# Optimization experiments

Measured on AMD Instinct MI355X. Metric: run time of the kernel, lower is better.

Reference implementation:

```python
import jax, jax.numpy as jnp
import numpy as np

N = 10000
E = 80000
NUM_TYPES = 1000
IN_CH = 64
EMB = 128
IN_GNN = EMB + IN_CH - 1  # 191
NUM_GRAPHS = 16
NUM_CLASSES = 2


def _glorot(key, shape):
    fan_in, fan_out = shape[0], shape[1]
    lim = jnp.sqrt(6.0 / (fan_in + fan_out))
    return jax.random.uniform(key, shape, jnp.float32, -lim, lim)


def setup_inputs() -> dict:
    key = jax.random.key(0)
    ks = jax.random.split(key, 20)
    node_type_ids = jax.random.randint(ks[0], (N,), 0, NUM_TYPES)
    other_feats = jax.random.normal(ks[1], (N, IN_CH - 1), jnp.float32)
    edge_index = jax.random.randint(ks[2], (2, E), 0, N)
    batch = jnp.sort(jax.random.randint(ks[3], (N,), 0, NUM_GRAPHS))
    params = dict(
        emb=jax.random.normal(ks[4], (NUM_TYPES, EMB), jnp.float32),
        W1=_glorot(ks[5], (IN_GNN, 2048)), b1=jnp.zeros((2048,), jnp.float32),
        W2=_glorot(ks[6], (2048, 1024)), b2=jnp.zeros((1024,), jnp.float32),
        W3=_glorot(ks[7], (1024, 1024)), b3=jnp.zeros((1024,), jnp.float32),
        h1w=_glorot(ks[8], (1024, 1024)), h1b=jnp.zeros((1024,), jnp.float32),
        h2w=_glorot(ks[9], (1024, 1024)), h2b=jnp.zeros((1024,), jnp.float32),
        h3w=_glorot(ks[10], (1024, 512)), h3b=jnp.zeros((512,), jnp.float32),
        ow=_glorot(ks[11], (512, NUM_CLASSES)), ob=jnp.zeros((NUM_CLASSES,), jnp.float32),
    )
    return dict(node_type_ids=node_type_ids, other_feats=other_feats,
                edge_index=edge_index, batch=batch, **params)


def _gcn_norm(edge_index, num_nodes):
    # add self loops + symmetric normalization D^-1/2 (A+I) D^-1/2 (PyG GCNConv defaults)
    loop = jnp.arange(num_nodes, dtype=edge_index.dtype)
    src = jnp.concatenate([edge_index[0], loop])
    dst = jnp.concatenate([edge_index[1], loop])
    deg = jax.ops.segment_sum(jnp.ones_like(src, jnp.float32), dst, num_segments=num_nodes)
    dinv = jnp.where(deg > 0, jax.lax.rsqrt(jnp.maximum(deg, 1.0)), 0.0)
    norm = dinv[src] * dinv[dst]
    return src, dst, norm


def _gcn_conv(x, src, dst, norm, W, b):
    h = x @ W                                    # [N, out] dense GEMM first (PyG order)
    msg = h[src] * norm[:, None]                 # gather + scale over edges
    agg = jax.ops.segment_sum(msg, dst, num_segments=x.shape[0])  # scatter-add
    return agg + b


def reference(node_type_ids, other_feats, edge_index, batch,
              emb, W1, b1, W2, b2, W3, b3,
              h1w, h1b, h2w, h2b, h3w, h3b, ow, ob):
    # eval mode: dropout is identity
    x = jnp.concatenate([emb[node_type_ids], other_feats], axis=-1)  # [N, 191]
    src, dst, norm = _gcn_norm(edge_index, x.shape[0])
    x = jax.nn.relu(_gcn_conv(x, src, dst, norm, W1, b1))
    x = jax.nn.relu(_gcn_conv(x, src, dst, norm, W2, b2))
    x = jax.nn.relu(_gcn_conv(x, src, dst, norm, W3, b3))
    # global mean pool over graphs
    sums = jax.ops.segment_sum(x, batch, num_segments=NUM_GRAPHS)
    cnts = jax.ops.segment_sum(jnp.ones((x.shape[0],), jnp.float32), batch, num_segments=NUM_GRAPHS)
    g = sums / jnp.maximum(cnts, 1.0)[:, None]   # [G, 1024]
    g = jax.nn.relu(g @ h1w + h1b)
    g = jax.nn.relu(g @ h2w + h2b)
    g = jax.nn.relu(g @ h3w + h3b)
    return g @ ow + ob                           # [G, num_classes]
```

## Files before the change

kernel.cpp:

```cpp
#include <hip/hip_runtime.h>


#define N_NODES 10000
#define N_EDGES 80000
#define EMB_DIM 128
#define FEAT_DIM 63
#define IN_GNN 191
#define IN_STRIDE 192
#define H1 2048
#define H2 1024
#define NGRAPH 16
#define NCLS 2
#define PCHUNK 8

using ushort = unsigned short;
typedef __attribute__((ext_vector_type(8))) short s8b;
typedef __attribute__((ext_vector_type(4))) float f4v;

__device__ __forceinline__ float us2f(ushort u) {
    union { unsigned int i; float f; } v; v.i = ((unsigned int)u) << 16; return v.f;
}
__device__ __forceinline__ ushort f2us(float f) {
    union { unsigned int i; float f; } v; v.f = f;
    unsigned int r = v.i + 0x7FFFu + ((v.i >> 16) & 1u);
    return (ushort)(r >> 16);
}
__device__ __forceinline__ float ldm(const void* p, long i, int md) {
    return (md == 1) ? us2f(((const ushort*)p)[i]) : ((const float*)p)[i];
}

__global__ void GraphV1EmbLarge_73864847556672_kernel() {}

__global__ void k_prep0(int* __restrict__ a, int na, float* __restrict__ b, int nb,
                        const ushort* __restrict__ feats, int* __restrict__ mode) {
    int i = blockIdx.x * 256 + threadIdx.x;
    if (i < na) a[i] = 0;
    if (i < nb) b[i] = 0.f;
    if (blockIdx.x == 0 && threadIdx.x == 0) {
        int sane = 0;
        for (int j = 0; j < 256; j++) {
            ushort u = feats[j];
            int e = (u >> 7) & 0xFF;
            if (u == 0 || (e >= 97 && e <= 157)) sane++;
        }
        *mode = (sane >= 220) ? 1 : 2;
    }
}

__global__ void k_deg_i(const int* __restrict__ dst, int* __restrict__ cnt) {
    int e = blockIdx.x * blockDim.x + threadIdx.x;
    if (e < N_EDGES) atomicAdd(&cnt[dst[e]], 1);
}
__global__ void k_scan(const int* __restrict__ cnt, int* __restrict__ indptr,
                       float* __restrict__ dinv) {
    __shared__ int part[256];
    int t = threadIdx.x;
    int base = t * 40;
    int s = 0;
    for (int i = 0; i < 40; i++) { int idx = base + i; if (idx < N_NODES) s += cnt[idx]; }
    part[t] = s;
    __syncthreads();
    if (t == 0) {
        int run = 0;
        for (int i = 0; i < 256; i++) { int tmp = part[i]; part[i] = run; run += tmp; }
        indptr[N_NODES] = run;
    }
    __syncthreads();
    int run = part[t];
    for (int i = 0; i < 40; i++) {
        int idx = base + i;
        if (idx < N_NODES) {
            indptr[idx] = run; run += cnt[idx];
            dinv[idx] = rsqrtf((float)cnt[idx] + 1.0f);
        }
    }
}
__global__ void k_fill(const int* __restrict__ src, const int* __restrict__ dst,
                       const int* __restrict__ indptr, int* __restrict__ cursor,
                       const float* __restrict__ dinv, int* __restrict__ ecol,
                       float* __restrict__ ewgt, const int* __restrict__ batch,
                       int* __restrict__ starts) {
    int b = blockIdx.x;
    if (b < 313) {
        int e = b * 256 + threadIdx.x;
        if (e >= N_EDGES) return;
        int d = dst[e], s = src[e];
        int slot = indptr[d] + atomicAdd(&cursor[d], 1);
        ecol[slot] = s;
        ewgt[slot] = dinv[s] * dinv[d];
    } else {
        int i = (b - 313) * 256 + threadIdx.x;
        if (i > N_NODES) return;
        int bc = (i < N_NODES) ? batch[i] : NGRAPH;
        int bp = (i == 0) ? -1 : batch[i - 1];
        for (int g = bp + 1; g <= bc; g++) starts[g] = i;
    }
}

__device__ __forceinline__ void cvt_tile(const void* W, int K, int N, int Kp,
                                         ushort* Wt, int n0, int k0, int md) {
    __shared__ float tile[32][33];
    int tx = threadIdx.x, ty = threadIdx.y;
    for (int r = ty; r < 32; r += 8) {
        int k = k0 + r;
        tile[r][tx] = (k < K) ? ldm(W, (long)k * N + n0 + tx, md) : 0.f;
    }
    __syncthreads();
    for (int r = ty; r < 32; r += 8) {
        int nn = n0 + r, kk = k0 + tx;
        if (kk < Kp) Wt[(long)nn * Kp + kk] = f2us(tile[tx][r]);
    }
}

__global__ void k_cvt_all(const void* W1, const void* W2, const void* W3,
                          const void* h1, const void* h2, const void* h3,
                          ushort* W1t, ushort* W2t, ushort* W3t,
                          ushort* h1t, ushort* h2t, ushort* h3t,
                          const int* __restrict__ types, const void* emb,
                          const void* feats, ushort* __restrict__ x0,
                          const void* b1, const void* b2, const void* b3,
                          float* __restrict__ b1f, float* __restrict__ b2f,
                          float* __restrict__ b3f, const int* __restrict__ mode) {
    int md = *mode;
    int b = blockIdx.x;
    if (b < 384) {
        int t = b;        cvt_tile(W1, IN_GNN, H1, IN_STRIDE, W1t, (t % 64) * 32, (t / 64) * 32, md);
    } else if (b < 2432) {
        int t = b - 384;  cvt_tile(W2, H1, H2, H1, W2t, (t % 32) * 32, (t / 32) * 32, md);
    } else if (b < 3456) {
        int t = b - 2432; cvt_tile(W3, H2, H2, H2, W3t, (t % 32) * 32, (t / 32) * 32, md);
    } else if (b < 4480) {
        int t = b - 3456; cvt_tile(h1, H2, H2, H2, h1t, (t % 32) * 32, (t / 32) * 32, md);
    } else if (b < 5504) {
        int t = b - 4480; cvt_tile(h2, H2, H2, H2, h2t, (t % 32) * 32, (t / 32) * 32, md);
    } else if (b < 6016) {
        int t = b - 5504; cvt_tile(h3, H2, 512, H2, h3t, (t % 16) * 32, (t / 16) * 32, md);
    } else if (b < 16016) {
        int i = b - 6016;
        int c = threadIdx.y * 32 + threadIdx.x;
        if (c >= IN_STRIDE) return;
        float v = 0.f;
        if (c < EMB_DIM) v = ldm(emb, (long)types[i] * EMB_DIM + c, md);
        else if (c < IN_GNN) v = ldm(feats, (long)i * FEAT_DIM + (c - EMB_DIM), md);
        x0[(long)i * IN_STRIDE + c] = f2us(v);
    } else {
        int i = (b - 16016) * 256 + threadIdx.y * 32 + threadIdx.x;
        if (i < 2048) b1f[i] = ldm(b1, i, md);
        else if (i < 3072) b2f[i - 2048] = ldm(b2, (long)(i - 2048), md);
        else if (i < 4096) b3f[i - 3072] = ldm(b3, (long)(i - 3072), md);
    }
}

__global__ void k_gather192(const ushort* __restrict__ H, const int* __restrict__ indptr,
                            const int* __restrict__ ecol, const float* __restrict__ ewgt,
                            const float* __restrict__ dinv, ushort* __restrict__ X) {
    int d = blockIdx.x;
    int c = threadIdx.x;
    float ds = dinv[d];
    float acc = us2f(H[(long)d * IN_STRIDE + c]) * ds * ds;
    int s0 = indptr[d], s1 = indptr[d + 1];
    int s = s0;
    for (; s + 1 < s1; s += 2) {
        int sa = ecol[s], sb = ecol[s + 1];
        float wa = ewgt[s], wb = ewgt[s + 1];
        float fa = us2f(H[(long)sa * IN_STRIDE + c]);
        float fb = us2f(H[(long)sb * IN_STRIDE + c]);
        acc += fa * wa + fb * wb;
    }
    if (s < s1) acc += us2f(H[(long)ecol[s] * IN_STRIDE + c]) * ewgt[s];
    X[(long)d * IN_STRIDE + c] = f2us(acc);
}

__device__ __forceinline__ void unpack8(uint4 u, float* f) {
    f[0] = us2f((ushort)(u.x & 0xffff)); f[1] = us2f((ushort)(u.x >> 16));
    f[2] = us2f((ushort)(u.y & 0xffff)); f[3] = us2f((ushort)(u.y >> 16));
    f[4] = us2f((ushort)(u.z & 0xffff)); f[5] = us2f((ushort)(u.z >> 16));
    f[6] = us2f((ushort)(u.w & 0xffff)); f[7] = us2f((ushort)(u.w >> 16));
}

__global__ void k_gather1024(const ushort* __restrict__ H, const int* __restrict__ indptr,
                             const int* __restrict__ ecol, const float* __restrict__ ewgt,
                             const float* __restrict__ dinv, const float* __restrict__ bias,
                             ushort* __restrict__ X) {
    int d = blockIdx.x;
    int c8 = threadIdx.x * 8;
    float ds = dinv[d];
    float a[8], f0[8], f1[8];
    unpack8(*(const uint4*)&H[(long)d * H2 + c8], a);
    float w0 = ds * ds;
#pragma unroll
    for (int r = 0; r < 8; r++) a[r] *= w0;
    int s0 = indptr[d], s1 = indptr[d + 1];
    int s = s0;
    for (; s + 1 < s1; s += 2) {
        int sa = ecol[s], sb = ecol[s + 1];
        float wa = ewgt[s], wb = ewgt[s + 1];
        uint4 ua = *(const uint4*)&H[(long)sa * H2 + c8];
        uint4 ub = *(const uint4*)&H[(long)sb * H2 + c8];
        unpack8(ua, f0);
        unpack8(ub, f1);
#pragma unroll
        for (int r = 0; r < 8; r++) a[r] += f0[r] * wa + f1[r] * wb;
    }
    if (s < s1) {
        uint4 ua = *(const uint4*)&H[(long)ecol[s] * H2 + c8];
        float wa = ewgt[s];
        unpack8(ua, f0);
#pragma unroll
        for (int r = 0; r < 8; r++) a[r] += f0[r] * wa;
    }
    uint4 o;
    unsigned int p0 = (unsigned int)f2us(fmaxf(a[0] + bias[c8 + 0], 0.f));
    unsigned int p1 = (unsigned int)f2us(fmaxf(a[1] + bias[c8 + 1], 0.f));
    unsigned int p2 = (unsigned int)f2us(fmaxf(a[2] + bias[c8 + 2], 0.f));
    unsigned int p3 = (unsigned int)f2us(fmaxf(a[3] + bias[c8 + 3], 0.f));
    unsigned int p4 = (unsigned int)f2us(fmaxf(a[4] + bias[c8 + 4], 0.f));
    unsigned int p5 = (unsigned int)f2us(fmaxf(a[5] + bias[c8 + 5], 0.f));
    unsigned int p6 = (unsigned int)f2us(fmaxf(a[6] + bias[c8 + 6], 0.f));
    unsigned int p7 = (unsigned int)f2us(fmaxf(a[7] + bias[c8 + 7], 0.f));
    o.x = p0 | (p1 << 16); o.y = p2 | (p3 << 16);
    o.z = p4 | (p5 << 16); o.w = p6 | (p7 << 16);
    *(uint4*)&X[(long)d * H2 + c8] = o;
}

__global__ __launch_bounds__(256) void k_mfma_gemm(
    const ushort* __restrict__ A, int lda, int M,
    const ushort* __restrict__ Wt, int K, int N,
    const float* __restrict__ bias, int relu,
    ushort* __restrict__ C, int NB) {
    __shared__ ushort As[2][128 * 32];
    __shared__ ushort Bs[2][128 * 32];
    int L = blockIdx.x;
    int i = L >> 3;
    int m_t = (L & 7) + (i / NB) * 8;
    int n_t = i % NB;
    int m0 = m_t * 128, n0 = n_t * 128;
    if (m0 >= M) return;
    int tid = threadIdx.x;
    int wave = tid >> 6, lane = tid & 63;
    int wm = (wave & 1) * 64, wn = (wave >> 1) * 64;
    int quad = lane >> 4, l16 = lane & 15;
    int srow = tid >> 2;
    int scol = (tid & 3) * 8;
    int swz = ((srow >> 1) & 3) << 3;
    int rwz = ((l16 >> 1) & 3) << 3;
    int wa0 = srow * 32 + (scol ^ swz);
    int wa1 = (64 + srow) * 32 + (scol ^ swz);

    f4v acc[4][4];
#pragma unroll
    for (int ii = 0; ii < 4; ii++)
#pragma unroll
        for (int jj = 0; jj < 4; jj++) acc[ii][jj] = (f4v)(0.f);

    int gm1 = m0 + srow;       if (gm1 >= M) gm1 = M - 1;
    int gm2 = m0 + 64 + srow;  if (gm2 >= M) gm2 = M - 1;
    const ushort* pa1 = A + (long)gm1 * lda + scol;
    const ushort* pa2 = A + (long)gm2 * lda + scol;
    const ushort* pb1 = Wt + (long)(n0 + srow) * K + scol;
    const ushort* pb2 = Wt + (long)(n0 + 64 + srow) * K + scol;

    int niter = K >> 5;
    s8b va1 = *(const s8b*)pa1;
    s8b va2 = *(const s8b*)pa2;
    s8b vb1 = *(const s8b*)pb1;
    s8b vb2 = *(const s8b*)pb2;
    *(s8b*)&As[0][wa0] = va1;
    *(s8b*)&As[0][wa1] = va2;
    *(s8b*)&Bs[0][wa0] = vb1;
    *(s8b*)&Bs[0][wa1] = vb2;
    if (niter > 1) {
        pa1 += 32; pa2 += 32; pb1 += 32; pb2 += 32;
        va1 = *(const s8b*)pa1;
        va2 = *(const s8b*)pa2;
        vb1 = *(const s8b*)pb1;
        vb2 = *(const s8b*)pb2;
    }

    for (int it = 0; it < niter; it++) {
        int cur = it & 1;
        __syncthreads();
        if (it + 1 < niter) {
            int nxt = cur ^ 1;
            *(s8b*)&As[nxt][wa0] = va1;
            *(s8b*)&As[nxt][wa1] = va2;
            *(s8b*)&Bs[nxt][wa0] = vb1;
            *(s8b*)&Bs[nxt][wa1] = vb2;
            if (it + 2 < niter) {
                pa1 += 32; pa2 += 32; pb1 += 32; pb2 += 32;
                va1 = *(const s8b*)pa1;
                va2 = *(const s8b*)pa2;
                vb1 = *(const s8b*)pb1;
                vb2 = *(const s8b*)pb2;
            }
        }
        s8b a[4], b[4];
#pragma unroll
        for (int ii = 0; ii < 4; ii++)
            a[ii] = *(const s8b*)&As[cur][(wm + ii * 16 + l16) * 32 + (quad * 8 ^ rwz)];
#pragma unroll
        for (int jj = 0; jj < 4; jj++)
            b[jj] = *(const s8b*)&Bs[cur][(wn + jj * 16 + l16) * 32 + (quad * 8 ^ rwz)];
#pragma unroll
        for (int ii = 0; ii < 4; ii++)
#pragma unroll
            for (int jj = 0; jj < 4; jj++)
                acc[ii][jj] = __builtin_amdgcn_mfma_f32_16x16x32_bf16(a[ii], b[jj], acc[ii][jj], 0, 0, 0);
    }

#pragma unroll
    for (int ii = 0; ii < 4; ii++) {
        int row0 = m0 + wm + ii * 16 + quad * 4;
#pragma unroll
        for (int jj = 0; jj < 4; jj++) {
            int colc = n0 + wn + jj * 16 + l16;
            float bv = bias ? bias[colc] : 0.f;
#pragma unroll
            for (int r = 0; r < 4; r++) {
                int row = row0 + r;
                if (row < M) {
                    float v = acc[ii][jj][r] + bv;
                    if (relu) v = fmaxf(v, 0.f);
                    C[(long)row * N + colc] = f2us(v);
                }
            }
        }
    }
}

__global__ void k_pool_part(const ushort* __restrict__ x, const int* __restrict__ starts,
                            float* __restrict__ acc) {
    int g = blockIdx.x / PCHUNK, ch = blockIdx.x % PCHUNK;
    int c = blockIdx.y * 256 + threadIdx.x;
    int s0 = starts[g], s1 = starts[g + 1];
    int len = s1 - s0;
    int per = (len + PCHUNK - 1) / PCHUNK;
    int r0 = s0 + ch * per;
    int r1 = r0 + per; if (r1 > s1) r1 = s1;
    if (r0 >= r1) return;
    float sum = 0.f;
    for (int i = r0; i < r1; i++) sum += us2f(x[(long)i * H2 + c]);
    atomicAdd(&acc[g * H2 + c], sum);
}

__global__ __launch_bounds__(256) void k_head_mfma_pool(const float* __restrict__ pacc,
                                                        const int* __restrict__ starts,
                                                        const ushort* __restrict__ Wt,
                                                        float* __restrict__ pt, int N) {
    __shared__ float red[4][16][16];
    int n0 = blockIdx.x * 16;
    int ks = blockIdx.y;
    int wave = threadIdx.x >> 6, lane = threadIdx.x & 63;
    int l16 = lane & 15, quad = lane >> 4;
    int cnt = starts[l16 + 1] - starts[l16];
    float rc = 1.f / (float)(cnt > 0 ? cnt : 1);
    int kbase = ks * 256 + wave * 64;
    f4v acc = (f4v)(0.f);
#pragma unroll
    for (int kk = 0; kk < 64; kk += 32) {
        int k = kbase + kk + quad * 8;
        s8b a;
        short* ap = (short*)&a;
#pragma unroll
        for (int j = 0; j < 8; j++) ap[j] = (short)f2us(pacc[l16 * 1024 + k + j] * rc);
        s8b b = *(const s8b*)&Wt[(long)(n0 + l16) * 1024 + k];
        acc = __builtin_amdgcn_mfma_f32_16x16x32_bf16(a, b, acc, 0, 0, 0);
    }
#pragma unroll
    for (int r = 0; r < 4; r++) red[wave][quad * 4 + r][l16] = acc[r];
    __syncthreads();
    int row = threadIdx.x >> 4, col = threadIdx.x & 15;
    float s = red[0][row][col] + red[1][row][col] + red[2][row][col] + red[3][row][col];
    pt[((long)ks * 16 + row) * N + n0 + col] = s;
}

__global__ __launch_bounds__(256) void k_head_mfma(const ushort* __restrict__ A,
                                                   const ushort* __restrict__ Wt,
                                                   float* __restrict__ pt, int N) {
    __shared__ float red[4][16][16];
    int n0 = blockIdx.x * 16;
    int ks = blockIdx.y;
    int wave = threadIdx.x >> 6, lane = threadIdx.x & 63;
    int l16 = lane & 15, quad = lane >> 4;
    int kbase = ks * 256 + wave * 64;
    f4v acc = (f4v)(0.f);
#pragma unroll
    for (int kk = 0; kk < 64; kk += 32) {
        int k = kbase + kk + quad * 8;
        s8b a = *(const s8b*)&A[l16 * 1024 + k];
        s8b b = *(const s8b*)&Wt[(long)(n0 + l16) * 1024 + k];
        acc = __builtin_amdgcn_mfma_f32_16x16x32_bf16(a, b, acc, 0, 0, 0);
    }
#pragma unroll
    for (int r = 0; r < 4; r++) red[wave][quad * 4 + r][l16] = acc[r];
    __syncthreads();
    int row = threadIdx.x >> 4, col = threadIdx.x & 15;
    float s = red[0][row][col] + red[1][row][col] + red[2][row][col] + red[3][row][col];
    pt[((long)ks * 16 + row) * N + n0 + col] = s;
}

__global__ void k_head_red(const float* __restrict__ pt, const void* __restrict__ bias,
                           ushort* __restrict__ out, int N,
                           const int* __restrict__ mode) {
    int md = *mode;
    int idx = blockIdx.x * 256 + threadIdx.x;
    if (idx >= 16 * N) return;
    int row = idx / N, col = idx - row * N;
    float s = pt[((long)0 * 16 + row) * N + col] + pt[((long)1 * 16 + row) * N + col]
            + pt[((long)2 * 16 + row) * N + col] + pt[((long)3 * 16 + row) * N + col];
    s = fmaxf(s + ldm(bias, (long)col, md), 0.f);
    out[(long)row * N + col] = f2us(s);
}

__global__ void k_head_out(const ushort* __restrict__ in, const void* __restrict__ W,
                           const void* __restrict__ b, void* __restrict__ out,
                           const int* __restrict__ mode) {
    int md = *mode;
    int row = blockIdx.x >> 1, cls = blockIdx.x & 1;
    int lane = threadIdx.x;
    float acc = 0.f;
    for (int k = lane; k < 512; k += 64)
        acc += us2f(in[row * 512 + k]) * ldm(W, (long)k * NCLS + cls, md);
#pragma unroll
    for (int off = 32; off > 0; off >>= 1) acc += __shfl_down(acc, off);
    if (lane == 0) {
        float v = acc + ldm(b, (long)cls, md);
        if (md == 1) ((ushort*)out)[row * NCLS + cls] = f2us(v);
        else ((float*)out)[row * NCLS + cls] = v;
    }
}

extern "C" void kernel_launch(void* const* d_in, const int* in_sizes, int n_in,
                              void* d_out, int out_size, void* d_ws, size_t ws_size,
                              hipStream_t stream) {
    static const int EXPECT[19] = {
        10000, 630000, 160000, 10000, 128000,
        391168, 2048, 2097152, 1024, 1048576, 1024,
        1048576, 1024, 1048576, 1024, 524288, 512, 1024, 2
    };
    if (n_in != 19) { hipMemsetAsync(d_out, 0x48, 64, stream); return; }
    for (int i = 0; i < 19; i++)
        if (in_sizes[i] != EXPECT[i]) { hipMemsetAsync(d_out, 0x50 + i, 64, stream); return; }
    if (ws_size < (size_t)90000000) { hipMemsetAsync(d_out, 0x49, 64, stream); return; }

    const int* node_types = (const int*)d_in[0];
    const void* other = d_in[1];
    const int* e_src = (const int*)d_in[2];
    const int* e_dst = e_src + N_EDGES;
    const int* batch = (const int*)d_in[3];

    char* w = (char*)d_ws;
    int* mode = (int*)w;      w += 256;
    int* cnt = (int*)w;       w += 10240 * 4;
    int* cursor = (int*)w;    w += 10240 * 4;
    float* dinv = (float*)w;  w += 10240 * 4;
    int* starts = (int*)w;    w += 256;
    int* indptr = (int*)w;    w += 10240 * 4;
    int* ecol = (int*)w;      w += 81920 * 4;
    float* ewgt = (float*)w;  w += 81920 * 4;
    float* b1f = (float*)w;   w += 2048 * 4;
    float* b2f = (float*)w;   w += 1024 * 4;
    float* b3f = (float*)w;   w += 1024 * 4;
    float* pt = (float*)w;    w += 4 * 16 * 1024 * 4;
    float* pacc = (float*)w;  w += 16 * 1024 * 4;
    ushort* hA = (ushort*)w;  w += 16 * 1024 * 2;
    ushort* hB = (ushort*)w;  w += 16 * 1024 * 2;
    ushort* x0 = (ushort*)w;  w += 1920000 * 2;
    ushort* A1 = (ushort*)w;  w += 1920000 * 2;
    ushort* W1t = (ushort*)w; w += 393216 * 2;
    ushort* W2t = (ushort*)w; w += 2097152 * 2;
    ushort* W3t = (ushort*)w; w += 1048576 * 2;
    ushort* h1wt = (ushort*)w; w += 1048576 * 2;
    ushort* h2wt = (ushort*)w; w += 1048576 * 2;
    ushort* h3wt = (ushort*)w; w += 524288 * 2;
    ushort* Hb = (ushort*)w;  w += 20480000 * 2;
    ushort* Gb = (ushort*)w;  w += 10240000 * 2;
    ushort* x2 = Hb;
    ushort* x3 = Hb + (size_t)N_NODES * H2;

    hipGetLastError();
    k_prep0<<<80, 256, 0, stream>>>(cnt, 20480, pacc, NGRAPH * H2, (const ushort*)other, mode);
    hipError_t e0 = hipGetLastError();
    if (e0 != hipSuccess) { hipMemsetAsync(d_out, 0x46, 64, stream); return; }
    k_deg_i<<<(N_EDGES + 255) / 256, 256, 0, stream>>>(e_dst, cnt);
    k_scan<<<1, 256, 0, stream>>>(cnt, indptr, dinv);
    k_fill<<<313 + 40, 256, 0, stream>>>(e_src, e_dst, indptr, cursor, dinv, ecol, ewgt, batch, starts);

    k_cvt_all<<<16032, dim3(32, 8), 0, stream>>>(d_in[5], d_in[7], d_in[9], d_in[11], d_in[13], d_in[15],
                                                 W1t, W2t, W3t, h1wt, h2wt, h3wt,
                                                 node_types, d_in[4], other, x0,
                                                 d_in[6], d_in[8], d_in[10], b1f, b2f, b3f, mode);

    k_gather192<<<N_NODES, IN_STRIDE, 0, stream>>>(x0, indptr, ecol, ewgt, dinv, A1);
    k_mfma_gemm<<<16 * 80, 256, 0, stream>>>(A1, IN_STRIDE, N_NODES, W1t, IN_STRIDE, H1, b1f, 1, Hb, 16);

    k_mfma_gemm<<<8 * 80, 256, 0, stream>>>(Hb, H1, N_NODES, W2t, H1, H2, nullptr, 0, Gb, 8);
    k_gather1024<<<N_NODES, 128, 0, stream>>>(Gb, indptr, ecol, ewgt, dinv, b2f, x2);

    k_mfma_gemm<<<8 * 80, 256, 0, stream>>>(x2, H2, N_NODES, W3t, H2, H2, nullptr, 0, Gb, 8);
    k_gather1024<<<N_NODES, 128, 0, stream>>>(Gb, indptr, ecol, ewgt, dinv, b3f, x3);

    k_pool_part<<<dim3(NGRAPH * PCHUNK, H2 / 256), 256, 0, stream>>>(x3, starts, pacc);

    k_head_mfma_pool<<<dim3(64, 4), 256, 0, stream>>>(pacc, starts, h1wt, pt, 1024);
    k_head_red<<<64, 256, 0, stream>>>(pt, d_in[12], hA, 1024, mode);
    k_head_mfma<<<dim3(64, 4), 256, 0, stream>>>(hA, h2wt, pt, 1024);
    k_head_red<<<64, 256, 0, stream>>>(pt, d_in[14], hB, 1024, mode);
    k_head_mfma<<<dim3(32, 4), 256, 0, stream>>>(hB, h3wt, pt, 512);
    k_head_red<<<32, 256, 0, stream>>>(pt, d_in[16], hA, 512, mode);
    k_head_out<<<NGRAPH * NCLS, 64, 0, stream>>>(hA, d_in[17], d_in[18], d_out, mode);

    hipError_t e1 = hipGetLastError();
    if (e1 != hipSuccess) hipMemsetAsync(d_out, 0x47, 64, stream);
}
```

Measured before the change: 401.9 us.

## Split 1024-wide gathers across column-slice blocks and fuse head split-K reductions

The 1024-column aggregation kernel now runs 8 blocks of 64 threads per node, each handling a 128-column slice with 4-byte loads, in place of one 128-thread block doing 16-byte loads. The aim is more blocks in flight to hide latency on the irregular neighbour reads. The cost is narrower memory transactions and the edge list being re-read once per slice. The MLP head layers drop their split-K partial buffer and separate reduce kernels: each block now covers the full K range with bias and ReLU fused, which removes three launches and the intermediate round trip but gives fewer blocks per layer.

```diff
diff --git a/kernel.cpp b/kernel.cpp
--- a/kernel.cpp
+++ b/kernel.cpp
@@ -171,56 +171,38 @@
     X[(long)d * IN_STRIDE + c] = f2us(acc);
 }
 
-__device__ __forceinline__ void unpack8(uint4 u, float* f) {
-    f[0] = us2f((ushort)(u.x & 0xffff)); f[1] = us2f((ushort)(u.x >> 16));
-    f[2] = us2f((ushort)(u.y & 0xffff)); f[3] = us2f((ushort)(u.y >> 16));
-    f[4] = us2f((ushort)(u.z & 0xffff)); f[5] = us2f((ushort)(u.z >> 16));
-    f[6] = us2f((ushort)(u.w & 0xffff)); f[7] = us2f((ushort)(u.w >> 16));
-}
-
-__global__ void k_gather1024(const ushort* __restrict__ H, const int* __restrict__ indptr,
-                             const int* __restrict__ ecol, const float* __restrict__ ewgt,
-                             const float* __restrict__ dinv, const float* __restrict__ bias,
-                             ushort* __restrict__ X) {
-    int d = blockIdx.x;
-    int c8 = threadIdx.x * 8;
+__global__ __launch_bounds__(64) void k_gather_slice(
+    const ushort* __restrict__ H, const int* __restrict__ indptr,
+    const int* __restrict__ ecol, const float* __restrict__ ewgt,
+    const float* __restrict__ dinv, const float* __restrict__ bias,
+    ushort* __restrict__ X) {
+    int L = blockIdx.x;
+    int d = L >> 3;
+    int c2 = (L & 7) * 128 + threadIdx.x * 2;
     float ds = dinv[d];
-    float a[8], f0[8], f1[8];
-    unpack8(*(const uint4*)&H[(long)d * H2 + c8], a);
     float w0 = ds * ds;
-#pragma unroll
-    for (int r = 0; r < 8; r++) a[r] *= w0;
+    unsigned int u = *(const unsigned int*)&H[(long)d * H2 + c2];
+    float a0 = us2f((ushort)(u & 0xffff)) * w0;
+    float a1 = us2f((ushort)(u >> 16)) * w0;
     int s0 = indptr[d], s1 = indptr[d + 1];
     int s = s0;
     for (; s + 1 < s1; s += 2) {
         int sa = ecol[s], sb = ecol[s + 1];
         float wa = ewgt[s], wb = ewgt[s + 1];
-        uint4 ua = *(const uint4*)&H[(long)sa * H2 + c8];
-        uint4 ub = *(const uint4*)&H[(long)sb * H2 + c8];
-        unpack8(ua, f0);
-        unpack8(ub, f1);
-#pragma unroll
-        for (int r = 0; r < 8; r++) a[r] += f0[r] * wa + f1[r] * wb;
+        unsigned int ua = *(const unsigned int*)&H[(long)sa * H2 + c2];
+        unsigned int ub = *(const unsigned int*)&H[(long)sb * H2 + c2];
+        a0 += us2f((ushort)(ua & 0xffff)) * wa + us2f((ushort)(ub & 0xffff)) * wb;
+        a1 += us2f((ushort)(ua >> 16)) * wa + us2f((ushort)(ub >> 16)) * wb;
     }
     if (s < s1) {
-        uint4 ua = *(const uint4*)&H[(long)ecol[s] * H2 + c8];
+        unsigned int ua = *(const unsigned int*)&H[(long)ecol[s] * H2 + c2];
         float wa = ewgt[s];
-        unpack8(ua, f0);
-#pragma unroll
-        for (int r = 0; r < 8; r++) a[r] += f0[r] * wa;
-    }
-    uint4 o;
-    unsigned int p0 = (unsigned int)f2us(fmaxf(a[0] + bias[c8 + 0], 0.f));
-    unsigned int p1 = (unsigned int)f2us(fmaxf(a[1] + bias[c8 + 1], 0.f));
-    unsigned int p2 = (unsigned int)f2us(fmaxf(a[2] + bias[c8 + 2], 0.f));
-    unsigned int p3 = (unsigned int)f2us(fmaxf(a[3] + bias[c8 + 3], 0.f));
-    unsigned int p4 = (unsigned int)f2us(fmaxf(a[4] + bias[c8 + 4], 0.f));
-    unsigned int p5 = (unsigned int)f2us(fmaxf(a[5] + bias[c8 + 5], 0.f));
-    unsigned int p6 = (unsigned int)f2us(fmaxf(a[6] + bias[c8 + 6], 0.f));
-    unsigned int p7 = (unsigned int)f2us(fmaxf(a[7] + bias[c8 + 7], 0.f));
-    o.x = p0 | (p1 << 16); o.y = p2 | (p3 << 16);
-    o.z = p4 | (p5 << 16); o.w = p6 | (p7 << 16);
-    *(uint4*)&X[(long)d * H2 + c8] = o;
+        a0 += us2f((ushort)(ua & 0xffff)) * wa;
+        a1 += us2f((ushort)(ua >> 16)) * wa;
+    }
+    unsigned int o = (unsigned int)f2us(fmaxf(a0 + bias[c2], 0.f))
+                   | ((unsigned int)f2us(fmaxf(a1 + bias[c2 + 1], 0.f)) << 16);
+    *(unsigned int*)&X[(long)d * H2 + c2] = o;
 }
 
 __global__ __launch_bounds__(256) void k_mfma_gemm(
@@ -343,21 +325,51 @@
     atomicAdd(&acc[g * H2 + c], sum);
 }
 
-__global__ __launch_bounds__(256) void k_head_mfma_pool(const float* __restrict__ pacc,
+__global__ __launch_bounds__(256) void k_head_full(const ushort* __restrict__ A,
+                                                   const ushort* __restrict__ Wt,
+                                                   const void* __restrict__ bias,
+                                                   ushort* __restrict__ out, int N,
+                                                   const int* __restrict__ mode) {
+    __shared__ float red[4][16][16];
+    int md = *mode;
+    int n0 = blockIdx.x * 16;
+    int wave = threadIdx.x >> 6, lane = threadIdx.x & 63;
+    int l16 = lane & 15, quad = lane >> 4;
+    int kbase = wave * 256;
+    f4v acc = (f4v)(0.f);
+#pragma unroll
+    for (int kk = 0; kk < 256; kk += 32) {
+        int k = kbase + kk + quad * 8;
+        s8b a = *(const s8b*)&A[l16 * 1024 + k];
+        s8b b = *(const s8b*)&Wt[(long)(n0 + l16) * 1024 + k];
+        acc = __builtin_amdgcn_mfma_f32_16x16x32_bf16(a, b, acc, 0, 0, 0);
+    }
+#pragma unroll
+    for (int r = 0; r < 4; r++) red[wave][quad * 4 + r][l16] = acc[r];
+    __syncthreads();
+    int row = threadIdx.x >> 4, col = threadIdx.x & 15;
+    float s = red[0][row][col] + red[1][row][col] + red[2][row][col] + red[3][row][col];
+    s = fmaxf(s + ldm(bias, (long)(n0 + col), md), 0.f);
+    out[(long)row * N + n0 + col] = f2us(s);
+}
+
+__global__ __launch_bounds__(256) void k_head_full_pool(const float* __restrict__ pacc,
                                                         const int* __restrict__ starts,
                                                         const ushort* __restrict__ Wt,
-                                                        float* __restrict__ pt, int N) {
+                                                        const void* __restrict__ bias,
+                                                        ushort* __restrict__ out, int N,
+                                                        const int* __restrict__ mode) {
     __shared__ float red[4][16][16];
+    int md = *mode;
     int n0 = blockIdx.x * 16;
-    int ks = blockIdx.y;
     int wave = threadIdx.x >> 6, lane = threadIdx.x & 63;
     int l16 = lane & 15, quad = lane >> 4;
     int cnt = starts[l16 + 1] - starts[l16];
     float rc = 1.f / (float)(cnt > 0 ? cnt : 1);
-    int kbase = ks * 256 + wave * 64;
+    int kbase = wave * 256;
     f4v acc = (f4v)(0.f);
 #pragma unroll
-    for (int kk = 0; kk < 64; kk += 32) {
+    for (int kk = 0; kk < 256; kk += 32) {
         int k = kbase + kk + quad * 8;
         s8b a;
         short* ap = (short*)&a;
@@ -371,45 +383,8 @@
     __syncthreads();
     int row = threadIdx.x >> 4, col = threadIdx.x & 15;
     float s = red[0][row][col] + red[1][row][col] + red[2][row][col] + red[3][row][col];
-    pt[((long)ks * 16 + row) * N + n0 + col] = s;
-}
-
-__global__ __launch_bounds__(256) void k_head_mfma(const ushort* __restrict__ A,
-                                                   const ushort* __restrict__ Wt,
-                                                   float* __restrict__ pt, int N) {
-    __shared__ float red[4][16][16];
-    int n0 = blockIdx.x * 16;
-    int ks = blockIdx.y;
-    int wave = threadIdx.x >> 6, lane = threadIdx.x & 63;
-    int l16 = lane & 15, quad = lane >> 4;
-    int kbase = ks * 256 + wave * 64;
-    f4v acc = (f4v)(0.f);
-#pragma unroll
-    for (int kk = 0; kk < 64; kk += 32) {
-        int k = kbase + kk + quad * 8;
-        s8b a = *(const s8b*)&A[l16 * 1024 + k];
-        s8b b = *(const s8b*)&Wt[(long)(n0 + l16) * 1024 + k];
-        acc = __builtin_amdgcn_mfma_f32_16x16x32_bf16(a, b, acc, 0, 0, 0);
-    }
-#pragma unroll
-    for (int r = 0; r < 4; r++) red[wave][quad * 4 + r][l16] = acc[r];
-    __syncthreads();
-    int row = threadIdx.x >> 4, col = threadIdx.x & 15;
-    float s = red[0][row][col] + red[1][row][col] + red[2][row][col] + red[3][row][col];
-    pt[((long)ks * 16 + row) * N + n0 + col] = s;
-}
-
-__global__ void k_head_red(const float* __restrict__ pt, const void* __restrict__ bias,
-                           ushort* __restrict__ out, int N,
-                           const int* __restrict__ mode) {
-    int md = *mode;
-    int idx = blockIdx.x * 256 + threadIdx.x;
-    if (idx >= 16 * N) return;
-    int row = idx / N, col = idx - row * N;
-    float s = pt[((long)0 * 16 + row) * N + col] + pt[((long)1 * 16 + row) * N + col]
-            + pt[((long)2 * 16 + row) * N + col] + pt[((long)3 * 16 + row) * N + col];
-    s = fmaxf(s + ldm(bias, (long)col, md), 0.f);
-    out[(long)row * N + col] = f2us(s);
+    s = fmaxf(s + ldm(bias, (long)(n0 + col), md), 0.f);
+    out[(long)row * N + n0 + col] = f2us(s);
 }
 
 __global__ void k_head_out(const ushort* __restrict__ in, const void* __restrict__ W,
@@ -461,7 +436,6 @@
     float* b1f = (float*)w;   w += 2048 * 4;
     float* b2f = (float*)w;   w += 1024 * 4;
     float* b3f = (float*)w;   w += 1024 * 4;
-    float* pt = (float*)w;    w += 4 * 16 * 1024 * 4;
     float* pacc = (float*)w;  w += 16 * 1024 * 4;
     ushort* hA = (ushort*)w;  w += 16 * 1024 * 2;
     ushort* hB = (ushort*)w;  w += 16 * 1024 * 2;
@@ -495,19 +469,16 @@
     k_mfma_gemm<<<16 * 80, 256, 0, stream>>>(A1, IN_STRIDE, N_NODES, W1t, IN_STRIDE, H1, b1f, 1, Hb, 16);
 
     k_mfma_gemm<<<8 * 80, 256, 0, stream>>>(Hb, H1, N_NODES, W2t, H1, H2, nullptr, 0, Gb, 8);
-    k_gather1024<<<N_NODES, 128, 0, stream>>>(Gb, indptr, ecol, ewgt, dinv, b2f, x2);
+    k_gather_slice<<<N_NODES * 8, 64, 0, stream>>>(Gb, indptr, ecol, ewgt, dinv, b2f, x2);
 
     k_mfma_gemm<<<8 * 80, 256, 0, stream>>>(x2, H2, N_NODES, W3t, H2, H2, nullptr, 0, Gb, 8);
-    k_gather1024<<<N_NODES, 128, 0, stream>>>(Gb, indptr, ecol, ewgt, dinv, b3f, x3);
+    k_gather_slice<<<N_NODES * 8, 64, 0, stream>>>(Gb, indptr, ecol, ewgt, dinv, b3f, x3);
 
     k_pool_part<<<dim3(NGRAPH * PCHUNK, H2 / 256), 256, 0, stream>>>(x3, starts, pacc);
 
-    k_head_mfma_pool<<<dim3(64, 4), 256, 0, stream>>>(pacc, starts, h1wt, pt, 1024);
-    k_head_red<<<64, 256, 0, stream>>>(pt, d_in[12], hA, 1024, mode);
-    k_head_mfma<<<dim3(64, 4), 256, 0, stream>>>(hA, h2wt, pt, 1024);
-    k_head_red<<<64, 256, 0, stream>>>(pt, d_in[14], hB, 1024, mode);
-    k_head_mfma<<<dim3(32, 4), 256, 0, stream>>>(hB, h3wt, pt, 512);
-    k_head_red<<<32, 256, 0, stream>>>(pt, d_in[16], hA, 512, mode);
+    k_head_full_pool<<<64, 256, 0, stream>>>(pacc, starts, h1wt, d_in[12], hA, 1024, mode);
+    k_head_full<<<64, 256, 0, stream>>>(hA, h2wt, d_in[14], hB, 1024, mode);
+    k_head_full<<<32, 256, 0, stream>>>(hB, h3wt, d_in[16], hA, 512, mode);
     k_head_out<<<NGRAPH * NCLS, 64, 0, stream>>>(hA, d_in[17], d_in[18], d_out, mode);
 
     hipError_t e1 = hipGetLastError();
```

After: 399.8 us. No clear change (-0.5%).
